# Performance work log

Hardware: AMD Instinct MI355X
Metric: run time of the kernel (lower is better)

## Reference

```python
import jax, jax.numpy as jnp
import numpy as np

N_FFT = 2048
HOP = 512
SR = 48000
T = 2_880_000  # 60 s stereo @ 48 kHz, multiple of HOP


def _hann(n):
    # torch.hann_window default (periodic=True)
    return (0.5 - 0.5 * jnp.cos(2.0 * jnp.pi * jnp.arange(n) / n)).astype(jnp.float32)


def _stft(x, win):
    # x: [C, T] -> [C, F, bins] complex64 (torch.stft center=True, reflect pad)
    pad = N_FFT // 2
    xp = jnp.pad(x, ((0, 0), (pad, pad)), mode='reflect')
    n_frames = 1 + (xp.shape[-1] - N_FFT) // HOP
    idx = jnp.arange(n_frames)[:, None] * HOP + jnp.arange(N_FFT)[None, :]
    frames = xp[:, idx] * win  # [C, F, N_FFT]
    return jnp.fft.rfft(frames, axis=-1)


def _istft(S, win, length):
    # S: [C, F, bins] -> [C, length]; overlap-add with window-square normalization
    frames = jnp.fft.irfft(S, n=N_FFT, axis=-1) * win  # [C, F, N_FFT]
    nF = frames.shape[1]
    total = (nF - 1) * HOP + N_FFT
    idx = jnp.arange(nF)[:, None] * HOP + jnp.arange(N_FFT)[None, :]
    ola = jnp.zeros((frames.shape[0], total), frames.dtype).at[:, idx].add(frames)
    wsum = jnp.zeros((total,), win.dtype).at[idx].add(jnp.broadcast_to(win ** 2, idx.shape))
    out = ola / jnp.where(wsum > 1e-11, wsum, 1.0)
    pad = N_FFT // 2
    return out[:, pad:pad + length]


def _eq_band(audio, freq, gain_db, q=1.0):
    win = _hann(N_FFT)
    S = _stft(audio, win)  # [C, F, bins]
    bins = S.shape[-1]
    freqs = jnp.linspace(0.0, 24000.0, bins)
    mask = jnp.exp(-((freqs - freq) / (freq / q)) ** 2)  # [bins]
    g_lin = 10.0 ** (gain_db / 20.0)
    S = S * (1.0 + (g_lin - 1.0) * mask)
    return _istft(S, win, audio.shape[-1])


def _compress(audio, threshold, ratio, attack, release, makeup_gain):
    aa = jnp.abs(audio) + 1e-8
    adb = 20.0 * jnp.log10(aa)
    gr = jnp.maximum(adb - threshold, 0.0) * (1.0 - 1.0 / ratio)  # [C, T]
    a_att = 1.0 - jnp.exp(-1.0 / (attack * SR))
    a_rel = 1.0 - jnp.exp(-1.0 / (release * SR))

    def step(prev, g):
        alpha = jnp.where(g > prev, a_att, a_rel)
        new = (1.0 - alpha) * prev + alpha * g
        return new, new

    init = jnp.zeros((audio.shape[0],), audio.dtype)
    _, gs = jax.lax.scan(step, init, gr[:, 1:].T)  # [T-1, C]
    gain_smooth = jnp.concatenate([init[:, None], gs.T], axis=1)  # [C, T]
    gain_lin = 10.0 ** ((-gain_smooth + makeup_gain) / 20.0)
    return jnp.sign(audio) * aa * gain_lin


def setup_inputs() -> dict:
    key = jax.random.key(0)
    audio = 0.1 * jax.random.normal(key, (2, T), dtype=jnp.float32)
    f32 = lambda v: jnp.float32(v)
    return {
        'audio': audio,
        'eq_low_gain': f32(3.0),
        'eq_low_mid_gain': f32(-2.0),
        'eq_high_mid_gain': f32(2.5),
        'eq_high_gain': f32(1.5),
        'comp_threshold': f32(-18.0),
        'comp_ratio': f32(4.0),
        'comp_attack': f32(0.01),
        'comp_release': f32(0.1),
        'comp_makeup_gain': f32(3.0),
        'saturation': f32(1.5),
    }


def reference(audio, eq_low_gain, eq_low_mid_gain, eq_high_mid_gain, eq_high_gain,
              comp_threshold, comp_ratio, comp_attack, comp_release,
              comp_makeup_gain, saturation):
    x = _eq_band(audio, 100.0, eq_low_gain)
    x = _eq_band(x, 500.0, eq_low_mid_gain)
    x = _eq_band(x, 3000.0, eq_high_mid_gain)
    x = _eq_band(x, 10000.0, eq_high_gain)
    x = _compress(x, comp_threshold, comp_ratio, comp_attack, comp_release, comp_makeup_gain)
    # saturation branch (original: python if on .item(); here jnp.where)
    return jnp.where(saturation > 1.0, jnp.tanh(x * saturation) / saturation, x)
```

## Files before the change

kernel.cpp:

```cpp
#include <hip/hip_runtime.h>
#include <math.h>

#define T_LEN   2880000
#define LASTFR  5625
#define NBLK_EQ 625
#define SEG     7680
#define NSEG    375
#define RECS    2560
#define ROWSA   2576
#define RST     384
#define PLANE   (ROWSA * RST)
#define SPLANE  (RECS * RST)

typedef float2 c2;
__device__ __forceinline__ c2 cadd(c2 a, c2 b){ return make_float2(a.x+b.x, a.y+b.y); }
__device__ __forceinline__ c2 csub(c2 a, c2 b){ return make_float2(a.x-b.x, a.y-b.y); }
__device__ __forceinline__ c2 cmul(c2 a, c2 b){ return make_float2(a.x*b.x - a.y*b.y, a.x*b.y + a.y*b.x); }
__device__ __forceinline__ c2 cmulj(c2 a, c2 b){ return make_float2(a.x*b.x + a.y*b.y, a.y*b.x - a.x*b.y); }

template<int SGN>
__device__ __forceinline__ void dft8(c2 v[8]) {
    const float r = 0.70710678118654752f;
    c2 t0 = cadd(v[0], v[4]), t1 = csub(v[0], v[4]);
    c2 t2 = cadd(v[2], v[6]), t3 = csub(v[2], v[6]);
    c2 u0 = cadd(v[1], v[5]), u1 = csub(v[1], v[5]);
    c2 u2 = cadd(v[3], v[7]), u3 = csub(v[3], v[7]);
    c2 t3r = (SGN < 0) ? make_float2(t3.y, -t3.x) : make_float2(-t3.y, t3.x);
    c2 u3r = (SGN < 0) ? make_float2(u3.y, -u3.x) : make_float2(-u3.y, u3.x);
    c2 E0 = cadd(t0, t2), E2 = csub(t0, t2);
    c2 E1 = cadd(t1, t3r), E3 = csub(t1, t3r);
    c2 O0 = cadd(u0, u2), O2 = csub(u0, u2);
    c2 O1 = cadd(u1, u3r), O3 = csub(u1, u3r);
    c2 O1w = (SGN < 0) ? make_float2(r*(O1.x+O1.y), r*(O1.y-O1.x))
                       : make_float2(r*(O1.x-O1.y), r*(O1.x+O1.y));
    c2 O2w = (SGN < 0) ? make_float2(O2.y, -O2.x) : make_float2(-O2.y, O2.x);
    c2 O3w = (SGN < 0) ? make_float2(r*(O3.y-O3.x), -r*(O3.x+O3.y))
                       : make_float2(-r*(O3.x+O3.y), r*(O3.x-O3.y));
    v[0] = cadd(E0, O0);  v[4] = csub(E0, O0);
    v[1] = cadd(E1, O1w); v[5] = csub(E1, O1w);
    v[2] = cadd(E2, O2w); v[6] = csub(E2, O2w);
    v[3] = cadd(E3, O3w); v[7] = csub(E3, O3w);
}

__device__ __forceinline__ c2 shx(c2 v, int m) {
    return make_float2(__shfl_xor(v.x, m), __shfl_xor(v.y, m));
}

__device__ __forceinline__ void emit_chunk(float* __restrict__ dst, const float* __restrict__ WN,
                                           int cchunk, int tid, c2 r0, c2 r1) {
    const bool edge = (cchunk <= 2) || (cchunk >= 5626);
    #pragma unroll
    for (int q = 0; q < 2; ++q) {
        c2 rr = (q == 0) ? r0 : r1;
        int m = cchunk * 512 + (q << 8) + tid;
        float inv = 0.66666666666667f;
        if (edge) {
            int tmn = (m >= 2048) ? (((m - 2048) >> 9) + 1) : 0;
            int tmx = min(LASTFR, m >> 9);
            float wsum = 0.0f;
            for (int tt = tmn; tt <= tmx; ++tt) {
                float w = WN[m - (tt << 9)];
                wsum += w * w;
            }
            inv = (wsum > 1e-11f) ? (1.0f / wsum) : 1.0f;
        }
        int o = m - 1024;
        dst[o]         = rr.x * inv;
        dst[T_LEN + o] = rr.y * inv;
    }
}

__global__ __launch_bounds__(256) void eq_band_kernel(
    const float* __restrict__ src, float* __restrict__ dst,
    const float* __restrict__ gain_db_p, const float f0)
{
    __shared__ c2 SA[2048];
    __shared__ c2 TWs1[2048];
    __shared__ c2 TWs2[256];
    __shared__ c2 TWs3[32];
    __shared__ float MKs[2048];
    __shared__ float WN[2048];

    const int tid = threadIdx.x;
    const int b   = blockIdx.x;

    const float gdb   = *gain_db_p;
    const float g_lin = exp2f(gdb * 0.16609640474436813f);
    const float gm1   = g_lin - 1.0f;

    const float st2048 = 6.283185307179586f / 2048.0f;
    for (int idx = tid; idx < 2048; idx += 256) {
        int m = idx >> 8, j = idx & 255;
        float ang = st2048 * (float)(j * m);
        TWs1[idx] = make_float2(cosf(ang), -sinf(ang));
        WN[idx] = 0.5f - 0.5f * cosf(st2048 * (float)idx);
        int tt = idx & 255;
        int bb = tt >> 2, jj = tt & 3;
        int qrev = ((jj & 1) << 1) | (jj >> 1);
        int k = (bb >> 3) + ((bb & 7) << 3) + (m << 6) + (qrev << 9);
        int kk = (k > 1024) ? (2048 - k) : k;
        float f = (float)kk * (24000.0f / 1024.0f);
        float d = (f - f0) / f0;
        MKs[idx] = (1.0f + gm1 * expf(-d * d)) * (1.0f / 2048.0f);
    }
    {
        int m = tid >> 5, j2 = tid & 31;
        float ang = (6.283185307179586f / 256.0f) * (float)(j2 * m);
        TWs2[tid] = make_float2(cosf(ang), -sinf(ang));
    }
    if (tid < 32) {
        int m = tid >> 2, j = tid & 3;
        float ang = (6.283185307179586f / 32.0f) * (float)(j * m);
        TWs3[tid] = make_float2(cosf(ang), -sinf(ang));
    }
    __syncthreads();

    const int t0   = max(0, 9 * b - 1);
    const int t1   = min(LASTFR, 9 * b + 10);
    const int cmin = 9 * b + 2;
    const int cmax = 9 * b + 10;

    c2 ring[8];
    #pragma unroll
    for (int q = 0; q < 8; ++q) ring[q] = make_float2(0.0f, 0.0f);

    for (int t = t0; t <= t1; ++t) {
        for (int j = tid; j < 2048; j += 256) {
            int ss = t * 512 + j - 1024;
            ss = (ss < 0) ? -ss : ss;
            ss = (ss >= T_LEN) ? (2 * T_LEN - 2 - ss) : ss;
            float w = WN[j];
            SA[j] = make_float2(src[ss] * w, src[T_LEN + ss] * w);
        }
        __syncthreads();

        c2 v[8];

        #pragma unroll
        for (int k = 0; k < 8; ++k) v[k] = SA[tid + (k << 8)];
        dft8<-1>(v);
        #pragma unroll
        for (int m = 1; m < 8; ++m) v[m] = cmul(v[m], TWs1[(m << 8) + tid]);
        #pragma unroll
        for (int m = 0; m < 8; ++m) SA[tid + (m << 8)] = v[m];
        __syncthreads();

        {
            int c = tid >> 5, j2 = tid & 31;
            int base = (c << 8) + j2;
            #pragma unroll
            for (int k = 0; k < 8; ++k) v[k] = SA[base + (k << 5)];
            dft8<-1>(v);
            #pragma unroll
            for (int m = 1; m < 8; ++m) v[m] = cmul(v[m], TWs2[(m << 5) + j2]);
            __syncthreads();
            #pragma unroll
            for (int m = 0; m < 8; ++m) SA[(c << 8) + (m << 5) + (j2 ^ (m << 2))] = v[m];
        }
        __syncthreads();

        {
            int bb = tid >> 2, j = tid & 3;
            int base = bb << 5, bx = (bb & 7) << 2;
            #pragma unroll
            for (int k = 0; k < 8; ++k) v[k] = SA[base + ((k << 2) ^ bx) + j];
            dft8<-1>(v);
            #pragma unroll
            for (int m = 1; m < 8; ++m) v[m] = cmul(v[m], TWs3[(m << 2) + j]);
            #pragma unroll
            for (int m = 0; m < 8; ++m) {
                c2 w = v[m];
                c2 p = shx(w, 2);
                c2 e  = (j & 2) ? csub(p, w) : cadd(w, p);
                c2 qq = shx(e, 1);
                c2 lo = (j & 1) ? csub(qq, e) : cadd(e, qq);
                c2 hi = (j & 1) ? make_float2(qq.x - e.y, qq.y + e.x)
                                : make_float2(e.x + qq.y, e.y - qq.x);
                w = (j & 2) ? hi : lo;
                float mk = MKs[(m << 8) + tid];
                w.x *= mk; w.y *= mk;
                c2 p2 = shx(w, 1);
                c2 e2 = (j & 1) ? csub(p2, w) : cadd(w, p2);
                c2 q2 = shx(e2, 2);
                c2 lo2 = (j & 1) ? make_float2(e2.x - q2.y, e2.y + q2.x)
                                 : cadd(e2, q2);
                c2 hi2 = (j & 1) ? make_float2(q2.x + e2.y, q2.y - e2.x)
                                 : csub(q2, e2);
                v[m] = (j & 2) ? hi2 : lo2;
            }
            #pragma unroll
            for (int m = 1; m < 8; ++m) v[m] = cmulj(v[m], TWs3[(m << 2) + j]);
            dft8<+1>(v);
            __syncthreads();
            #pragma unroll
            for (int k = 0; k < 8; ++k) SA[base + ((k << 2) ^ bx) + j] = v[k];
        }
        __syncthreads();

        {
            int c = tid >> 5, j2 = tid & 31;
            #pragma unroll
            for (int m = 0; m < 8; ++m) v[m] = SA[(c << 8) + (m << 5) + (j2 ^ (m << 2))];
            #pragma unroll
            for (int m = 1; m < 8; ++m) v[m] = cmulj(v[m], TWs2[(m << 5) + j2]);
            dft8<+1>(v);
            __syncthreads();
            #pragma unroll
            for (int k = 0; k < 8; ++k) SA[(c << 8) + (k << 5) + j2] = v[k];
        }
        __syncthreads();

        {
            #pragma unroll
            for (int m = 0; m < 8; ++m) v[m] = SA[tid + (m << 8)];
            #pragma unroll
            for (int m = 1; m < 8; ++m) v[m] = cmulj(v[m], TWs1[(m << 8) + tid]);
            dft8<+1>(v);
            #pragma unroll
            for (int k = 0; k < 8; ++k) {
                float w = WN[tid + (k << 8)];
                ring[k].x += v[k].x * w;
                ring[k].y += v[k].y * w;
            }
        }
        __syncthreads();

        if (t >= cmin) emit_chunk(dst, WN, t, tid, ring[0], ring[1]);
        #pragma unroll
        for (int q = 0; q < 6; ++q) ring[q] = ring[q + 2];
        ring[6] = make_float2(0.0f, 0.0f);
        ring[7] = make_float2(0.0f, 0.0f);
    }
    for (int c = t1 + 1; c <= cmax; ++c) {
        emit_chunk(dst, WN, c, tid, ring[0], ring[1]);
        #pragma unroll
        for (int q = 0; q < 6; ++q) ring[q] = ring[q + 2];
        ring[6] = make_float2(0.0f, 0.0f);
        ring[7] = make_float2(0.0f, 0.0f);
    }
}

__device__ __forceinline__ float gaval(float v, float thr, float coef) {
    float aa = fabsf(v) + 1e-8f;
    return fmaxf(6.020599913279624f * __log2f(aa) - thr, 0.0f) * coef;
}

__global__ __launch_bounds__(256) void triple_kernel(
    const float* __restrict__ y, float4* __restrict__ rec,
    const float* __restrict__ thr_p, const float* __restrict__ ratio_p,
    const float* __restrict__ att_p, const float* __restrict__ rel_p)
{
    __shared__ float4 L[64][33];
    const int r0 = blockIdx.x * 32;
    const int s0 = blockIdx.y * 64;
    const int c  = blockIdx.z;
    const int tid = threadIdx.x;

    float thr = *thr_p, ratio = *ratio_p;
    float A  = expf(-1.0f / ((*att_p) * 48000.0f));
    float Bc = expf(-1.0f / ((*rel_p) * 48000.0f));
    float ra = (1.0f - Bc) / (1.0f - A);
    float coef = (1.0f - 1.0f / ratio) * (1.0f - A);

    const int rr = tid & 31;
    #pragma unroll 1
    for (int it = 0; it < 8; ++it) {
        int ss = (tid >> 5) + it * 8;
        int s = s0 + ss;
        if (s < NSEG) {
            int li = s * SEG + 3 * (r0 + rr);
            const float* yp = y + c * T_LEN + li;
            float a1 = gaval(yp[0], thr, coef);
            float a2 = gaval(yp[1], thr, coef);
            float a3 = gaval(yp[2], thr, coef);
            if (li == 0) a1 = 0.0f;
            float b2 = ra * a2, b3 = ra * a3;
            float C0 = a1, C1 = ra * a1;
            float D0 = fmaf(A, C0, a2);
            float D1 = fmaxf(fmaf(A, C1, a2), fmaf(Bc, C0, b2));
            float D2 = fmaf(Bc, C1, b2);
            float I0 = fmaf(A, D0, a3);
            float I1 = fmaxf(fmaf(A, D1, a3), fmaf(Bc, D0, b3));
            float I2 = fmaxf(fmaf(A, D2, a3), fmaf(Bc, D1, b3));
            float I3 = fmaf(Bc, D2, b3);
            L[ss][rr] = make_float4(I0, I1, I2, I3);
        }
    }
    __syncthreads();
    const int cc = tid & 63;
    #pragma unroll 1
    for (int it = 0; it < 8; ++it) {
        int rr2 = (tid >> 6) + it * 4;
        if (s0 + cc < NSEG)
            rec[(long)c * PLANE + (r0 + rr2) * RST + 4 + s0 + cc] = L[cc][rr2];
    }
}

__global__ __launch_bounds__(256) void padzero_kernel(float4* __restrict__ rec)
{
    int idx = blockIdx.x * 256 + threadIdx.x;
    if (idx >= 2 * RECS * 4) return;
    int ch = idx / (RECS * 4);
    int r  = (idx >> 2) % RECS;
    int colp = idx & 3;
    rec[(long)ch * PLANE + r * RST + colp] = make_float4(0.f, 0.f, 0.f, 0.f);
}

template<bool STORE>
__device__ void scan_pass(const float4* __restrict__ cp, float* __restrict__ sp,
                          float& p, float S0, float S1, float S2, float S3)
{
    float4 bA[16], bB[16];
    #pragma unroll
    for (int k = 0; k < 16; ++k) bA[k] = cp[k * RST];
    __builtin_amdgcn_sched_barrier(0);
    int r = 0;
    #pragma unroll 1
    for (int gg = 0; gg < 80; ++gg) {
        #pragma unroll
        for (int k = 0; k < 16; ++k) bB[k] = cp[(r + 16 + k) * RST];
        __builtin_amdgcn_sched_barrier(0);
        #pragma unroll
        for (int k = 0; k < 16; ++k) {
            float4 v = bA[k];
            float t0 = fmaf(S0, p, v.x), t1 = fmaf(S1, p, v.y);
            float t2 = fmaf(S2, p, v.z), t3 = fmaf(S3, p, v.w);
            p = fmaxf(fmaxf(t0, t1), fmaxf(t2, t3));
            if (STORE) sp[(r + k) * RST] = p;
        }
        __builtin_amdgcn_sched_barrier(0);
        #pragma unroll
        for (int k = 0; k < 16; ++k) bA[k] = cp[(r + 32 + k) * RST];
        __builtin_amdgcn_sched_barrier(0);
        #pragma unroll
        for (int k = 0; k < 16; ++k) {
            float4 v = bB[k];
            float t0 = fmaf(S0, p, v.x), t1 = fmaf(S1, p, v.y);
            float t2 = fmaf(S2, p, v.z), t3 = fmaf(S3, p, v.w);
            p = fmaxf(fmaxf(t0, t1), fmaxf(t2, t3));
            if (STORE) sp[(r + 16 + k) * RST] = p;
        }
        __builtin_amdgcn_sched_barrier(0);
        r += 32;
    }
}

__global__ __launch_bounds__(64, 1) void scan_kernel(
    const float4* __restrict__ rec, float* __restrict__ gsP,
    const float* __restrict__ att_p, const float* __restrict__ rel_p)
{
    int gid = blockIdx.x * 64 + threadIdx.x;
    int g2 = min(gid, 2 * NSEG - 1);
    int c = g2 / NSEG;
    int s = g2 - c * NSEG;

    float A  = expf(-1.0f / ((*att_p) * 48000.0f));
    float Bc = expf(-1.0f / ((*rel_p) * 48000.0f));
    float S0 = A * A * A, S1 = A * A * Bc, S2 = A * Bc * Bc, S3 = Bc * Bc * Bc;

    const float4* cbase = rec + (long)c * PLANE + s;
    float* sbase = gsP + (long)c * SPLANE + 4 + s;
    float p = 0.0f;

    #pragma unroll 1
    for (int j = 0; j < 4; ++j)
        scan_pass<false>(cbase + j, nullptr, p, S0, S1, S2, S3);
    scan_pass<true>(cbase + 4, sbase, p, S0, S1, S2, S3);
}

__global__ __launch_bounds__(256) void final_kernel(
    const float* __restrict__ y, const float* __restrict__ gsP, float* __restrict__ out,
    const float* __restrict__ thr_p, const float* __restrict__ ratio_p,
    const float* __restrict__ att_p, const float* __restrict__ rel_p,
    const float* __restrict__ mk_p, const float* __restrict__ sat_p)
{
    __shared__ float LP[64][34];
    const int r0 = blockIdx.x * 32;
    const int s0 = blockIdx.y * 64;
    const int c  = blockIdx.z;
    const int tid = threadIdx.x;

    float thr = *thr_p, ratio = *ratio_p, mk = *mk_p, sat = *sat_p;
    float A  = expf(-1.0f / ((*att_p) * 48000.0f));
    float Bc = expf(-1.0f / ((*rel_p) * 48000.0f));
    float ra = (1.0f - Bc) / (1.0f - A);
    float coef = (1.0f - 1.0f / ratio) * (1.0f - A);
    const float* gb = gsP + (long)c * SPLANE;

    for (int idx = tid; idx < 33 * 64; idx += 256) {
        int rr = idx >> 6, ss = idx & 63;
        int s = s0 + ss;
        float v = 0.0f;
        if (s < NSEG) {
            int row = r0 - 1 + rr;
            if (row >= 0)      v = gb[row * RST + 4 + s];
            else if (s > 0)    v = gb[(RECS - 1) * RST + 4 + s - 1];
        }
        LP[ss][rr] = v;
    }
    __syncthreads();

    #pragma unroll 1
    for (int it = 0; it < 8; ++it) {
        int idx = it * 256 + tid;
        int ss = idx >> 5, rr = idx & 31;
        int s = s0 + ss;
        if (s >= NSEG) continue;
        int r = r0 + rr;
        int li = s * SEG + 3 * r;
        const float* yp = y + c * T_LEN + li;
        float* op = out + c * T_LEN + li;
        float p = LP[ss][rr];
        float y0 = yp[0], y1 = yp[1], y2 = yp[2];
        #pragma unroll
        for (int q = 0; q < 3; ++q) {
            float v = (q == 0) ? y0 : ((q == 1) ? y1 : y2);
            float a = gaval(v, thr, coef);
            if (li + q == 0) a = 0.0f;
            p = fmaxf(fmaf(A, p, a), fmaf(Bc, p, ra * a));
            float aa = fabsf(v) + 1e-8f;
            float gl = exp2f((mk - p) * 0.16609640474436813f);
            float ro = aa * gl;
            ro = (v < 0.0f) ? -ro : ro;
            if (sat > 1.0f) ro = tanhf(ro * sat) / sat;
            op[q] = ro;
        }
    }
}

extern "C" void kernel_launch(void* const* d_in, const int* in_sizes, int n_in,
                              void* d_out, int out_size, void* d_ws, size_t ws_size,
                              hipStream_t stream)
{
    const float* audio = (const float*)d_in[0];
    const float* g1    = (const float*)d_in[1];
    const float* g2    = (const float*)d_in[2];
    const float* g3    = (const float*)d_in[3];
    const float* g4    = (const float*)d_in[4];
    const float* thr   = (const float*)d_in[5];
    const float* ratio = (const float*)d_in[6];
    const float* att   = (const float*)d_in[7];
    const float* rel   = (const float*)d_in[8];
    const float* mkup  = (const float*)d_in[9];
    const float* sat   = (const float*)d_in[10];

    float* out  = (float*)d_out;
    float* bufA = (float*)d_ws;
    float4* rec = (float4*)(bufA + 2 * T_LEN);
    float*  gsP = (float*)(rec + 2 * (long)PLANE);

    eq_band_kernel<<<NBLK_EQ, 256, 0, stream>>>(audio, out,  g1, 100.0f);
    eq_band_kernel<<<NBLK_EQ, 256, 0, stream>>>(out,   bufA, g2, 500.0f);
    eq_band_kernel<<<NBLK_EQ, 256, 0, stream>>>(bufA,  out,  g3, 3000.0f);
    eq_band_kernel<<<NBLK_EQ, 256, 0, stream>>>(out,   bufA, g4, 10000.0f);

    padzero_kernel<<<(2 * RECS * 4 + 255) / 256, 256, 0, stream>>>(rec);
    dim3 tgrid(RECS / 32, (NSEG + 63) / 64, 2);
    triple_kernel<<<tgrid, 256, 0, stream>>>(bufA, rec, thr, ratio, att, rel);
    scan_kernel<<<12, 64, 0, stream>>>(rec, gsP, att, rel);
    final_kernel<<<tgrid, 256, 0, stream>>>(bufA, gsP, out,
                                            thr, ratio, att, rel, mkup, sat);
}
```

Baseline: 795.1 us.

## Compose 15-sample max-plus records instead of 3 to shorten serial scan

Each record in the compressor's max-plus envelope scan now covers 15 samples instead of 3, so a record carries 16 coefficients held in four float4 planes. The serial scan kernel then walks 512 rows per segment instead of 2560, cutting the length of the latency-bound sequential chain. The cost is quadratic work per record in the build kernel, 16 FMA/max terms per scan step, and a longer 15-step recurrence per thread in the final kernel.

```diff
diff --git a/kernel.cpp b/kernel.cpp
--- a/kernel.cpp
+++ b/kernel.cpp
@@ -6,11 +6,12 @@
 #define NBLK_EQ 625
 #define SEG     7680
 #define NSEG    375
-#define RECS    2560
-#define ROWSA   2576
+#define KREC    15
+#define NREC    512
+#define PROWS   528
 #define RST     384
-#define PLANE   (ROWSA * RST)
-#define SPLANE  (RECS * RST)
+#define PL      (PROWS * RST)
+#define SPL     (NREC * RST)
 
 typedef float2 c2;
 __device__ __forceinline__ c2 cadd(c2 a, c2 b){ return make_float2(a.x+b.x, a.y+b.y); }
@@ -245,12 +246,12 @@
     return fmaxf(6.020599913279624f * __log2f(aa) - thr, 0.0f) * coef;
 }
 
-__global__ __launch_bounds__(256) void triple_kernel(
+__global__ __launch_bounds__(256) void rec15_kernel(
     const float* __restrict__ y, float4* __restrict__ rec,
     const float* __restrict__ thr_p, const float* __restrict__ ratio_p,
     const float* __restrict__ att_p, const float* __restrict__ rel_p)
 {
-    __shared__ float4 L[64][33];
+    __shared__ float4 Lsub[32][9][4];
     const int r0 = blockIdx.x * 32;
     const int s0 = blockIdx.y * 64;
     const int c  = blockIdx.z;
@@ -262,86 +263,111 @@
     float ra = (1.0f - Bc) / (1.0f - A);
     float coef = (1.0f - 1.0f / ratio) * (1.0f - A);
 
-    const int rr = tid & 31;
+    const int rr = tid & 31, cg = tid >> 5;
+    const int orow = tid >> 3, oc8 = tid & 7;
+
     #pragma unroll 1
     for (int it = 0; it < 8; ++it) {
-        int ss = (tid >> 5) + it * 8;
-        int s = s0 + ss;
+        int s = s0 + it * 8 + cg;
         if (s < NSEG) {
-            int li = s * SEG + 3 * (r0 + rr);
-            const float* yp = y + c * T_LEN + li;
-            float a1 = gaval(yp[0], thr, coef);
-            float a2 = gaval(yp[1], thr, coef);
-            float a3 = gaval(yp[2], thr, coef);
-            if (li == 0) a1 = 0.0f;
-            float b2 = ra * a2, b3 = ra * a3;
-            float C0 = a1, C1 = ra * a1;
-            float D0 = fmaf(A, C0, a2);
-            float D1 = fmaxf(fmaf(A, C1, a2), fmaf(Bc, C0, b2));
-            float D2 = fmaf(Bc, C1, b2);
-            float I0 = fmaf(A, D0, a3);
-            float I1 = fmaxf(fmaf(A, D1, a3), fmaf(Bc, D0, b3));
-            float I2 = fmaxf(fmaf(A, D2, a3), fmaf(Bc, D1, b3));
-            float I3 = fmaf(Bc, D2, b3);
-            L[ss][rr] = make_float4(I0, I1, I2, I3);
-        }
-    }
-    __syncthreads();
-    const int cc = tid & 63;
-    #pragma unroll 1
-    for (int it = 0; it < 8; ++it) {
-        int rr2 = (tid >> 6) + it * 4;
-        if (s0 + cc < NSEG)
-            rec[(long)c * PLANE + (r0 + rr2) * RST + 4 + s0 + cc] = L[cc][rr2];
+            int r = r0 + rr;
+            int li = s * SEG + KREC * r;
+            const float* yp = y + (long)c * T_LEN + li;
+            float I[16];
+            float a = gaval(yp[0], thr, coef);
+            if (li == 0) a = 0.0f;
+            I[0] = a; I[1] = ra * a;
+            #pragma unroll
+            for (int n = 1; n < KREC; ++n) {
+                a = gaval(yp[n], thr, coef);
+                float b = ra * a;
+                I[n + 1] = fmaf(Bc, I[n], b);
+                #pragma unroll
+                for (int j = n; j >= 1; --j)
+                    I[j] = fmaxf(fmaf(A, I[j], a), fmaf(Bc, I[j - 1], b));
+                I[0] = fmaf(A, I[0], a);
+            }
+            Lsub[rr][cg][0] = make_float4(I[0],  I[1],  I[2],  I[3]);
+            Lsub[rr][cg][1] = make_float4(I[4],  I[5],  I[6],  I[7]);
+            Lsub[rr][cg][2] = make_float4(I[8],  I[9],  I[10], I[11]);
+            Lsub[rr][cg][3] = make_float4(I[12], I[13], I[14], I[15]);
+        }
+        __syncthreads();
+        int so = s0 + it * 8 + oc8;
+        if (so < NSEG) {
+            #pragma unroll
+            for (int q = 0; q < 4; ++q)
+                rec[(long)(c * 4 + q) * PL + (r0 + orow) * RST + 4 + so]
+                    = Lsub[orow][oc8][q];
+        }
+        __syncthreads();
     }
 }
 
 __global__ __launch_bounds__(256) void padzero_kernel(float4* __restrict__ rec)
 {
     int idx = blockIdx.x * 256 + threadIdx.x;
-    if (idx >= 2 * RECS * 4) return;
-    int ch = idx / (RECS * 4);
-    int r  = (idx >> 2) % RECS;
-    int colp = idx & 3;
-    rec[(long)ch * PLANE + r * RST + colp] = make_float4(0.f, 0.f, 0.f, 0.f);
+    if (idx >= 8 * NREC * 4) return;
+    int colp  = idx & 3;
+    int r     = (idx >> 2) & (NREC - 1);
+    int plane = idx >> 11;
+    rec[(long)plane * PL + r * RST + colp] = make_float4(0.f, 0.f, 0.f, 0.f);
+}
+
+struct Rec { float4 a, b, c, d; };
+
+__device__ __forceinline__ void load8(Rec (&bb)[8],
+    const float4* p0, const float4* p1, const float4* p2, const float4* p3, int r)
+{
+    #pragma unroll
+    for (int k = 0; k < 8; ++k) {
+        int o = (r + k) * RST;
+        bb[k].a = p0[o]; bb[k].b = p1[o]; bb[k].c = p2[o]; bb[k].d = p3[o];
+    }
 }
 
 template<bool STORE>
-__device__ void scan_pass(const float4* __restrict__ cp, float* __restrict__ sp,
-                          float& p, float S0, float S1, float S2, float S3)
-{
-    float4 bA[16], bB[16];
+__device__ __forceinline__ void consume8(Rec (&bb)[8], float* sp, int r, float& p,
+                                         const float (&S)[16])
+{
     #pragma unroll
-    for (int k = 0; k < 16; ++k) bA[k] = cp[k * RST];
+    for (int k = 0; k < 8; ++k) {
+        Rec v = bb[k];
+        float m0 = fmaxf(fmaf(S[0],  p, v.a.x), fmaf(S[1],  p, v.a.y));
+        float m1 = fmaxf(fmaf(S[2],  p, v.a.z), fmaf(S[3],  p, v.a.w));
+        float m2 = fmaxf(fmaf(S[4],  p, v.b.x), fmaf(S[5],  p, v.b.y));
+        float m3 = fmaxf(fmaf(S[6],  p, v.b.z), fmaf(S[7],  p, v.b.w));
+        float m4 = fmaxf(fmaf(S[8],  p, v.c.x), fmaf(S[9],  p, v.c.y));
+        float m5 = fmaxf(fmaf(S[10], p, v.c.z), fmaf(S[11], p, v.c.w));
+        float m6 = fmaxf(fmaf(S[12], p, v.d.x), fmaf(S[13], p, v.d.y));
+        float m7 = fmaxf(fmaf(S[14], p, v.d.z), fmaf(S[15], p, v.d.w));
+        m0 = fmaxf(m0, m1); m2 = fmaxf(m2, m3);
+        m4 = fmaxf(m4, m5); m6 = fmaxf(m6, m7);
+        m0 = fmaxf(m0, m2); m4 = fmaxf(m4, m6);
+        p = fmaxf(m0, m4);
+        if (STORE) sp[(r + k) * RST] = p;
+    }
+}
+
+template<bool STORE>
+__device__ void scan_pass(const float4* p0, const float4* p1, const float4* p2,
+                          const float4* p3, float* sp, float& p, const float (&S)[16])
+{
+    Rec bA[8], bB[8];
+    load8(bA, p0, p1, p2, p3, 0);
     __builtin_amdgcn_sched_barrier(0);
     int r = 0;
     #pragma unroll 1
-    for (int gg = 0; gg < 80; ++gg) {
-        #pragma unroll
-        for (int k = 0; k < 16; ++k) bB[k] = cp[(r + 16 + k) * RST];
+    for (int gg = 0; gg < NREC / 16; ++gg) {
+        load8(bB, p0, p1, p2, p3, r + 8);
         __builtin_amdgcn_sched_barrier(0);
-        #pragma unroll
-        for (int k = 0; k < 16; ++k) {
-            float4 v = bA[k];
-            float t0 = fmaf(S0, p, v.x), t1 = fmaf(S1, p, v.y);
-            float t2 = fmaf(S2, p, v.z), t3 = fmaf(S3, p, v.w);
-            p = fmaxf(fmaxf(t0, t1), fmaxf(t2, t3));
-            if (STORE) sp[(r + k) * RST] = p;
-        }
+        consume8<STORE>(bA, sp, r, p, S);
         __builtin_amdgcn_sched_barrier(0);
-        #pragma unroll
-        for (int k = 0; k < 16; ++k) bA[k] = cp[(r + 32 + k) * RST];
+        load8(bA, p0, p1, p2, p3, r + 16);
         __builtin_amdgcn_sched_barrier(0);
-        #pragma unroll
-        for (int k = 0; k < 16; ++k) {
-            float4 v = bB[k];
-            float t0 = fmaf(S0, p, v.x), t1 = fmaf(S1, p, v.y);
-            float t2 = fmaf(S2, p, v.z), t3 = fmaf(S3, p, v.w);
-            p = fmaxf(fmaxf(t0, t1), fmaxf(t2, t3));
-            if (STORE) sp[(r + 16 + k) * RST] = p;
-        }
+        consume8<STORE>(bB, sp, r + 8, p, S);
         __builtin_amdgcn_sched_barrier(0);
-        r += 32;
+        r += 16;
     }
 }
 
@@ -356,16 +382,34 @@
 
     float A  = expf(-1.0f / ((*att_p) * 48000.0f));
     float Bc = expf(-1.0f / ((*rel_p) * 48000.0f));
-    float S0 = A * A * A, S1 = A * A * Bc, S2 = A * Bc * Bc, S3 = Bc * Bc * Bc;
-
-    const float4* cbase = rec + (long)c * PLANE + s;
-    float* sbase = gsP + (long)c * SPLANE + 4 + s;
+    float S[16];
+    {
+        float pa = 1.0f;
+        #pragma unroll
+        for (int j = 15; j >= 0; --j) { S[j] = pa; pa *= A; }
+        float pb = 1.0f;
+        #pragma unroll
+        for (int j = 0; j < 16; ++j) { S[j] *= pb; pb *= Bc; }
+    }
+
+    float* sbase = gsP + (long)c * SPL + 4 + s;
     float p = 0.0f;
 
     #pragma unroll 1
-    for (int j = 0; j < 4; ++j)
-        scan_pass<false>(cbase + j, nullptr, p, S0, S1, S2, S3);
-    scan_pass<true>(cbase + 4, sbase, p, S0, S1, S2, S3);
+    for (int j = 0; j < 4; ++j) {
+        const float4* p0 = rec + (long)(c * 4 + 0) * PL + s + j;
+        const float4* p1 = rec + (long)(c * 4 + 1) * PL + s + j;
+        const float4* p2 = rec + (long)(c * 4 + 2) * PL + s + j;
+        const float4* p3 = rec + (long)(c * 4 + 3) * PL + s + j;
+        scan_pass<false>(p0, p1, p2, p3, nullptr, p, S);
+    }
+    {
+        const float4* p0 = rec + (long)(c * 4 + 0) * PL + s + 4;
+        const float4* p1 = rec + (long)(c * 4 + 1) * PL + s + 4;
+        const float4* p2 = rec + (long)(c * 4 + 2) * PL + s + 4;
+        const float4* p3 = rec + (long)(c * 4 + 3) * PL + s + 4;
+        scan_pass<true>(p0, p1, p2, p3, sbase, p, S);
+    }
 }
 
 __global__ __launch_bounds__(256) void final_kernel(
@@ -385,7 +429,7 @@
     float Bc = expf(-1.0f / ((*rel_p) * 48000.0f));
     float ra = (1.0f - Bc) / (1.0f - A);
     float coef = (1.0f - 1.0f / ratio) * (1.0f - A);
-    const float* gb = gsP + (long)c * SPLANE;
+    const float* gb = gsP + (long)c * SPL;
 
     for (int idx = tid; idx < 33 * 64; idx += 256) {
         int rr = idx >> 6, ss = idx & 63;
@@ -394,7 +438,7 @@
         if (s < NSEG) {
             int row = r0 - 1 + rr;
             if (row >= 0)      v = gb[row * RST + 4 + s];
-            else if (s > 0)    v = gb[(RECS - 1) * RST + 4 + s - 1];
+            else if (s > 0)    v = gb[(NREC - 1) * RST + 4 + s - 1];
         }
         LP[ss][rr] = v;
     }
@@ -407,14 +451,13 @@
         int s = s0 + ss;
         if (s >= NSEG) continue;
         int r = r0 + rr;
-        int li = s * SEG + 3 * r;
-        const float* yp = y + c * T_LEN + li;
-        float* op = out + c * T_LEN + li;
+        int li = s * SEG + KREC * r;
+        const float* yp = y + (long)c * T_LEN + li;
+        float* op = out + (long)c * T_LEN + li;
         float p = LP[ss][rr];
-        float y0 = yp[0], y1 = yp[1], y2 = yp[2];
-        #pragma unroll
-        for (int q = 0; q < 3; ++q) {
-            float v = (q == 0) ? y0 : ((q == 1) ? y1 : y2);
+        #pragma unroll
+        for (int q = 0; q < KREC; ++q) {
+            float v = yp[q];
             float a = gaval(v, thr, coef);
             if (li + q == 0) a = 0.0f;
             p = fmaxf(fmaf(A, p, a), fmaf(Bc, p, ra * a));
@@ -447,16 +490,16 @@
     float* out  = (float*)d_out;
     float* bufA = (float*)d_ws;
     float4* rec = (float4*)(bufA + 2 * T_LEN);
-    float*  gsP = (float*)(rec + 2 * (long)PLANE);
+    float*  gsP = (float*)(rec + 8 * (long)PL);
 
     eq_band_kernel<<<NBLK_EQ, 256, 0, stream>>>(audio, out,  g1, 100.0f);
     eq_band_kernel<<<NBLK_EQ, 256, 0, stream>>>(out,   bufA, g2, 500.0f);
     eq_band_kernel<<<NBLK_EQ, 256, 0, stream>>>(bufA,  out,  g3, 3000.0f);
     eq_band_kernel<<<NBLK_EQ, 256, 0, stream>>>(out,   bufA, g4, 10000.0f);
 
-    padzero_kernel<<<(2 * RECS * 4 + 255) / 256, 256, 0, stream>>>(rec);
-    dim3 tgrid(RECS / 32, (NSEG + 63) / 64, 2);
-    triple_kernel<<<tgrid, 256, 0, stream>>>(bufA, rec, thr, ratio, att, rel);
+    padzero_kernel<<<(8 * NREC * 4 + 255) / 256, 256, 0, stream>>>(rec);
+    dim3 tgrid(NREC / 32, (NSEG + 63) / 64, 2);
+    rec15_kernel<<<tgrid, 256, 0, stream>>>(bufA, rec, thr, ratio, att, rel);
     scan_kernel<<<12, 64, 0, stream>>>(rec, gsP, att, rel);
     final_kernel<<<tgrid, 256, 0, stream>>>(bufA, gsP, out,
                                             thr, ratio, att, rel, mkup, sat);
```

Measured after the change: 767.0 us. -3.5%, faster.
